# Optimization experiments

Measured on AMD Instinct MI355X. Metric: run time of the kernel, lower is better.

## Reference

```python
import jax, jax.numpy as jnp
import numpy as np

B, S, D = 2, 2048, 1024
H, DK, DV = 16, 64, 64
DF = 4096
EPS = 1e-5


def _layer_norm(x, g, b):
    mu = jnp.mean(x, axis=-1, keepdims=True)
    var = jnp.mean((x - mu) ** 2, axis=-1, keepdims=True)
    return (x - mu) * jax.lax.rsqrt(var + EPS) * g + b


def setup_inputs() -> dict:
    key = jax.random.key(0)
    ks = jax.random.split(key, 12)
    s = lambda fan_in: 1.0 / np.sqrt(fan_in)
    return {
        "enc_input": jax.random.normal(ks[0], (B, S, D), dtype=jnp.float32),
        "wq": jax.random.uniform(ks[1], (D, H * DK), jnp.float32, -s(D), s(D)),
        "wk": jax.random.uniform(ks[2], (D, H * DK), jnp.float32, -s(D), s(D)),
        "wv": jax.random.uniform(ks[3], (D, H * DV), jnp.float32, -s(D), s(D)),
        "wo": jax.random.uniform(ks[4], (H * DV, D), jnp.float32, -s(H * DV), s(H * DV)),
        "w1": jax.random.uniform(ks[5], (D, DF), jnp.float32, -s(D), s(D)),
        "b1": jax.random.uniform(ks[6], (DF,), jnp.float32, -s(D), s(D)),
        "w2": jax.random.uniform(ks[7], (DF, D), jnp.float32, -s(DF), s(DF)),
        "b2": jax.random.uniform(ks[8], (D,), jnp.float32, -s(DF), s(DF)),
        "ln1_g": jnp.ones((D,), jnp.float32),
        "ln1_b": jnp.zeros((D,), jnp.float32),
        "ln2_g": jnp.ones((D,), jnp.float32),
        "ln2_b": jnp.zeros((D,), jnp.float32),
    }


def reference(enc_input, wq, wk, wv, wo, w1, b1, w2, b2, ln1_g, ln1_b, ln2_g, ln2_b):
    x = enc_input
    # QKV projections -> [B, H, S, d]
    q = (x @ wq).reshape(B, S, H, DK).transpose(0, 2, 1, 3)
    k = (x @ wk).reshape(B, S, H, DK).transpose(0, 2, 1, 3)
    v = (x @ wv).reshape(B, S, H, DV).transpose(0, 2, 1, 3)
    # scaled dot-product attention (scale = 1/sqrt(d_k), dropout is identity at eval)
    score = jnp.einsum("bhqd,bhkd->bhqk", q, k) / jnp.sqrt(jnp.float32(DK))
    attn = jax.nn.softmax(score, axis=-1)
    ctx = jnp.einsum("bhqk,bhkd->bhqd", attn, v)
    ctx = ctx.transpose(0, 2, 1, 3).reshape(B, S, H * DV)
    atn_out = ctx @ wo
    # Add & Norm 1
    h = _layer_norm(x + atn_out, ln1_g, ln1_b)
    # FFN
    ffn = jax.nn.relu(h @ w1 + b1) @ w2 + b2
    # Add & Norm 2
    return _layer_norm(h + ffn, ln2_g, ln2_b)
```

## Files before the change

kernel.cpp:

```cpp
#include <hip/hip_runtime.h>
#include <hip/hip_bf16.h>

typedef __bf16 bf16;
typedef __bf16 bf16x4 __attribute__((ext_vector_type(4)));
typedef __bf16 bf16x8 __attribute__((ext_vector_type(8)));
typedef float  f32x4  __attribute__((ext_vector_type(4)));

#define KB 2
#define KS 2048
#define KD 1024
#define KH 16
#define KM (KB*KS)
#define KQKVN 3072
#define KDF 4096

__device__ __forceinline__ f32x4 mfma16(bf16x8 a, bf16x8 b, f32x4 c) {
  return __builtin_amdgcn_mfma_f32_16x16x32_bf16(a, b, c, 0, 0, 0);
}

__device__ __forceinline__ void g2l16(const bf16* g, bf16* l) {
  __builtin_amdgcn_global_load_lds(
      (const __attribute__((address_space(1))) unsigned int*)g,
      (__attribute__((address_space(3))) unsigned int*)l, 16, 0, 0);
}

__global__ __launch_bounds__(256) void cvt_bf16_kernel(const float* __restrict__ in,
                                                       bf16* __restrict__ out, int n) {
  int i = (blockIdx.x * 256 + threadIdx.x) * 4;
  if (i >= n) return;
  f32x4 v = *reinterpret_cast<const f32x4*>(in + i);
  bf16x4 o;
  o[0] = (bf16)v[0]; o[1] = (bf16)v[1]; o[2] = (bf16)v[2]; o[3] = (bf16)v[3];
  *reinterpret_cast<bf16x4*>(out + i) = o;
}

__global__ __launch_bounds__(256) void wtrans_kernel(const float* __restrict__ W,
                                                     bf16* __restrict__ WT,
                                                     int K, int N) {
  __shared__ float tile[32][33];
  const int n0 = blockIdx.x * 32, k0 = blockIdx.y * 32;
  const int tx = threadIdx.x & 31, ty = threadIdx.x >> 5;
#pragma unroll
  for (int j = ty; j < 32; j += 8) tile[j][tx] = W[(size_t)(k0 + j) * N + n0 + tx];
  __syncthreads();
#pragma unroll
  for (int j = ty; j < 32; j += 8) WT[(size_t)(n0 + j) * K + k0 + tx] = (bf16)tile[tx][j];
}

__global__ __launch_bounds__(256) void kvpack_kernel(const bf16* __restrict__ qkv,
                                                     bf16* __restrict__ kp,
                                                     bf16* __restrict__ vt) {
  __shared__ bf16 tile[64][72];
  const int s0 = blockIdx.x * 64;
  const int bh = blockIdx.y;
  const int b = bh >> 4, h = bh & 15;
  const int t = threadIdx.x;
  const int r = t >> 3, c8 = (t & 7) * 8;
#pragma unroll
  for (int rr = r; rr < 64; rr += 32) {
    const size_t grow = (size_t)(b * KS + s0 + rr) * KQKVN + h * 64 + c8;
    bf16x8 kv = *reinterpret_cast<const bf16x8*>(&qkv[grow + 1024]);
    *reinterpret_cast<bf16x8*>(&kp[((size_t)bh * KS + s0 + rr) * 64 + c8]) = kv;
    bf16x8 vv = *reinterpret_cast<const bf16x8*>(&qkv[grow + 2048]);
#pragma unroll
    for (int j = 0; j < 8; j++) tile[rr][c8 + j] = vv[j];
  }
  __syncthreads();
#pragma unroll
  for (int dd = r; dd < 64; dd += 32) {
    bf16x8 v;
#pragma unroll
    for (int j = 0; j < 8; j++) {
      const int pi = c8 + j;
      v[j] = tile[((pi & 3) << 4) + (pi >> 2)][dd];
    }
    *reinterpret_cast<bf16x8*>(&vt[(size_t)bh * 64 * KS + (size_t)dd * KS + s0 + c8]) = v;
  }
}

struct P4 { bf16* p[4]; };

template <typename OUT_T, bool RELU, bool HAS_BIAS, bool SPLITK>
__global__ __launch_bounds__(512, 2) void gemm256(const bf16* __restrict__ A,
                                                  const bf16* __restrict__ BT,
                                                  OUT_T* __restrict__ C, P4 pr,
                                                  const float* __restrict__ bias,
                                                  int M, int N, int K, int Kslice) {
  extern __shared__ __align__(16) bf16 sm[];
  const int tid = threadIdx.x, lane = tid & 63, w = tid >> 6;
  const int wr = w >> 2, wc = w & 3;
  const int gx = gridDim.x;
  const int nwg = gx * gridDim.y;
  int flat = blockIdx.y * gx + blockIdx.x;
  flat = (flat & 7) * (nwg >> 3) + (flat >> 3);
  const int bn = (flat % gx) * 256;
  const int bm = (flat / gx) * 256;
  const int z = blockIdx.z;
  const int NT = (SPLITK ? Kslice : K) >> 5;
  const int lr = lane & 15, hi = lane >> 4;
  int srow[2], scol[2];
#pragma unroll
  for (int j = 0; j < 2; j++) {
    const int u = j * 512 + tid;
    srow[j] = u >> 2;
    scol[j] = (((u & 3) ^ ((u >> 2) & 3))) * 8;
  }
  const bf16* Abase = A + (size_t)bm * K + (SPLITK ? z * Kslice : 0);
  const bf16* Bbase = BT + (size_t)bn * K + (SPLITK ? z * Kslice : 0);
  auto stage = [&](int t) {
    bf16* dst = sm + (size_t)(t & 3) * 16384;
    const int k0 = t * 32;
#pragma unroll
    for (int j = 0; j < 2; j++) {
      g2l16(Abase + (size_t)srow[j] * K + k0 + scol[j], dst + (j * 512 + w * 64) * 8);
      g2l16(Bbase + (size_t)srow[j] * K + k0 + scol[j],
            dst + 8192 + (j * 512 + w * 64) * 8);
    }
  };
  f32x4 acc[8][4] = {};
  stage(0); stage(1); stage(2);
  for (int t = 0; t < NT; t++) {
    const int rem = NT - 1 - t;
    if (rem >= 2)      asm volatile("s_waitcnt vmcnt(8)" ::: "memory");
    else if (rem == 1) asm volatile("s_waitcnt vmcnt(4)" ::: "memory");
    else               asm volatile("s_waitcnt vmcnt(0)" ::: "memory");
    __builtin_amdgcn_sched_barrier(0);
    __builtin_amdgcn_s_barrier();
    __builtin_amdgcn_sched_barrier(0);
    if (t + 3 < NT) stage(t + 3);
    const bf16* sa = sm + (size_t)(t & 3) * 16384;
    const bf16* sb = sa + 8192;
    bf16x8 af[8], bfr[4];
#pragma unroll
    for (int mf = 0; mf < 8; mf++) {
      const int row = wr * 128 + mf * 16 + lr;
      af[mf] = *(const bf16x8*)&sa[row * 32 + ((hi ^ (row & 3)) * 8)];
    }
#pragma unroll
    for (int nf = 0; nf < 4; nf++) {
      const int row = wc * 64 + nf * 16 + lr;
      bfr[nf] = *(const bf16x8*)&sb[row * 32 + ((hi ^ (row & 3)) * 8)];
    }
    __builtin_amdgcn_s_setprio(1);
#pragma unroll
    for (int mf = 0; mf < 8; mf++)
#pragma unroll
      for (int nf = 0; nf < 4; nf++)
        acc[mf][nf] = mfma16(af[mf], bfr[nf], acc[mf][nf]);
    __builtin_amdgcn_s_setprio(0);
  }
  const int rg = hi * 4, cl = lr;
  if (SPLITK) {
    bf16* P = pr.p[z];
#pragma unroll
    for (int mf = 0; mf < 8; mf++)
#pragma unroll
      for (int nf = 0; nf < 4; nf++) {
        const int col = bn + wc * 64 + nf * 16 + cl;
#pragma unroll
        for (int i = 0; i < 4; i++) {
          const int row = bm + wr * 128 + mf * 16 + rg + i;
          P[(size_t)row * N + col] = (bf16)acc[mf][nf][i];
        }
      }
  } else {
#pragma unroll
    for (int mf = 0; mf < 8; mf++)
#pragma unroll
      for (int nf = 0; nf < 4; nf++) {
        const int col = bn + wc * 64 + nf * 16 + cl;
        float bv = 0.f;
        if (HAS_BIAS) bv = bias[col];
#pragma unroll
        for (int i = 0; i < 4; i++) {
          const int row = bm + wr * 128 + mf * 16 + rg + i;
          float v = acc[mf][nf][i] + bv;
          if (RELU) v = fmaxf(v, 0.f);
          C[(size_t)row * N + col] = (OUT_T)v;
        }
      }
  }
}

__global__ __launch_bounds__(256) void ffn2_reduce_kernel(const bf16* __restrict__ p0,
                                                          const bf16* __restrict__ p1,
                                                          const bf16* __restrict__ p2,
                                                          const bf16* __restrict__ p3,
                                                          const float* __restrict__ b2,
                                                          float* __restrict__ out) {
  const size_t i = ((size_t)blockIdx.x * 256 + threadIdx.x) * 8;
  bf16x8 a0 = *(const bf16x8*)(p0 + i);
  bf16x8 a1 = *(const bf16x8*)(p1 + i);
  bf16x8 a2 = *(const bf16x8*)(p2 + i);
  bf16x8 a3 = *(const bf16x8*)(p3 + i);
  const int col = (int)(i & (KD - 1));
  f32x4 b0 = *(const f32x4*)(b2 + col);
  f32x4 b1 = *(const f32x4*)(b2 + col + 4);
  f32x4 o0, o1;
#pragma unroll
  for (int j = 0; j < 4; j++)
    o0[j] = (float)a0[j] + (float)a1[j] + (float)a2[j] + (float)a3[j] + b0[j];
#pragma unroll
  for (int j = 0; j < 4; j++)
    o1[j] = (float)a0[j + 4] + (float)a1[j + 4] + (float)a2[j + 4] + (float)a3[j + 4] + b1[j];
  *(f32x4*)(out + i) = o0;
  *(f32x4*)(out + i + 4) = o1;
}

template <typename OUT_T, bool RELU, bool HAS_BIAS, int BN>
__global__ __launch_bounds__(256) void gemm_bt(const bf16* __restrict__ A,
                                               const bf16* __restrict__ BT,
                                               OUT_T* __restrict__ C,
                                               const float* __restrict__ bias,
                                               int M, int N, int K) {
  constexpr int NF = BN / 32;
  __shared__ __align__(16) bf16 sa[2][128 * 32];
  __shared__ __align__(16) bf16 sb[2][BN * 32];
  const int t = threadIdx.x, lane = t & 63, w = t >> 6;
  const int gx = gridDim.x;
  const int nwg = gx * gridDim.y;
  int flat = blockIdx.y * gx + blockIdx.x;
  if ((nwg & 7) == 0) flat = (flat & 7) * (nwg >> 3) + (flat >> 3);
  const int bn = (flat % gx) * BN;
  const int bm = (flat / gx) * 128;
  const int wr = w >> 1, wc = w & 1;
  const int wcol = wc * (BN / 2);
  const int lr = lane & 15, lk = (lane >> 4) * 8;
  const int srow = w * 16 + (lane >> 2);
  const int scol = (lane & 3) * 8;
  f32x4 acc[4][NF] = {};
  const int NT = K >> 5;
  auto stage = [&](int kt, int buf) {
#pragma unroll
    for (int i = 0; i < 2; i++)
      g2l16(A + (size_t)(bm + i * 64 + srow) * K + kt * 32 + scol,
            &sa[buf][(i * 64 + w * 16) * 32]);
#pragma unroll
    for (int i = 0; i < BN / 64; i++)
      g2l16(BT + (size_t)(bn + i * 64 + srow) * K + kt * 32 + scol,
            &sb[buf][(i * 64 + w * 16) * 32]);
  };
  stage(0, 0);
  int cur = 0;
  for (int kt = 0; kt < NT; kt++) {
    __syncthreads();
    if (kt + 1 < NT) stage(kt + 1, cur ^ 1);
    bf16x8 af[4], bfr[NF];
#pragma unroll
    for (int m = 0; m < 4; m++)
      af[m] = *(const bf16x8*)&sa[cur][(wr * 64 + m * 16 + lr) * 32 + lk];
#pragma unroll
    for (int n = 0; n < NF; n++)
      bfr[n] = *(const bf16x8*)&sb[cur][(wcol + n * 16 + lr) * 32 + lk];
#pragma unroll
    for (int m = 0; m < 4; m++)
#pragma unroll
      for (int n = 0; n < NF; n++)
        acc[m][n] = mfma16(af[m], bfr[n], acc[m][n]);
    cur ^= 1;
  }
  const int rg = (lane >> 4) * 4, cl = lane & 15;
#pragma unroll
  for (int m = 0; m < 4; m++)
#pragma unroll
    for (int n = 0; n < NF; n++) {
      const int col = bn + wcol + n * 16 + cl;
      float bv = 0.f;
      if (HAS_BIAS) bv = bias[col];
#pragma unroll
      for (int i = 0; i < 4; i++) {
        const int row = bm + wr * 64 + m * 16 + rg + i;
        float v = acc[m][n][i] + bv;
        if (RELU) v = fmaxf(v, 0.f);
        C[(size_t)row * N + col] = (OUT_T)v;
      }
    }
}

__global__ __launch_bounds__(256) void attn_kernel(const bf16* __restrict__ qkv,
                                                   const bf16* __restrict__ kp,
                                                   const bf16* __restrict__ vt,
                                                   bf16* __restrict__ ctx) {
  __shared__ __align__(16) bf16 ksm[4][64 * 64];
  __shared__ __align__(16) bf16 vsm[4][64 * 64];
  __shared__ __align__(16) bf16 psm[4][32 * 64];
  const int t = threadIdx.x, lane = t & 63, w = t >> 6;
  const int flat = blockIdx.y * 16 + blockIdx.x;
  const int xcd = flat & 7, jj = flat >> 3;
  const int bh = xcd + 8 * (jj >> 4);
  const int qb = jj & 15;
  const int b = bh >> 4, h = bh & 15;
  const int qbase = qb * 128 + w * 32;
  const int lr = lane & 15, hi = lane >> 4;
  const int lk = hi * 8, rg = hi * 4, cl = lr;

  bf16x8 aq[2][2];
#pragma unroll
  for (int m = 0; m < 2; m++)
#pragma unroll
    for (int kk = 0; kk < 2; kk++) {
      bf16x8 v = *reinterpret_cast<const bf16x8*>(
          &qkv[(size_t)(b * KS + qbase + m * 16 + lr) * KQKVN + h * 64 + kk * 32 + lk]);
#pragma unroll
      for (int e = 0; e < 8; e++) v[e] = (bf16)((float)v[e] * 0.125f);
      aq[m][kk] = v;
    }

  const bf16* kpb = kp + (size_t)bh * KS * 64;
  const bf16* vtb = vt + (size_t)bh * 64 * KS;

  auto stageKV = [&](int tt) {
    const int kt0 = tt * 64;
    bf16* kd = &ksm[tt & 3][0];
    bf16* vd = &vsm[tt & 3][0];
#pragma unroll
    for (int i = 0; i < 2; i++) {
      const int q = i * 4096 + w * 1024 + (lane << 4);
      const int row = q >> 7;
      const int slot = ((q >> 4) & 7) ^ (row & 7);
      g2l16(kpb + (size_t)(kt0 + row) * 64 + slot * 8, kd + ((i * 4096 + w * 1024) >> 1));
      g2l16(vtb + (size_t)row * KS + kt0 + slot * 8,   vd + ((i * 4096 + w * 1024) >> 1));
    }
  };

  f32x4 accd[2][4] = {};
  float lsum[2][4] = {};

  stageKV(0); stageKV(1); stageKV(2);
  char* pb = (char*)&psm[w][0];
  const int NT = KS / 64;
  for (int tt = 0; tt < NT; tt++) {
    const int rem = NT - 1 - tt;
    if (rem >= 2)      asm volatile("s_waitcnt vmcnt(8)" ::: "memory");
    else if (rem == 1) asm volatile("s_waitcnt vmcnt(4)" ::: "memory");
    else               asm volatile("s_waitcnt vmcnt(0)" ::: "memory");
    __builtin_amdgcn_sched_barrier(0);
    __builtin_amdgcn_s_barrier();
    __builtin_amdgcn_sched_barrier(0);
    if (tt + 3 < NT) stageKV(tt + 3);
    const char* kb = (const char*)&ksm[tt & 3][0];
    const char* vb = (const char*)&vsm[tt & 3][0];
    bf16x8 bk[4][2];
#pragma unroll
    for (int n = 0; n < 4; n++)
#pragma unroll
      for (int kk = 0; kk < 2; kk++) {
        const int row = n * 16 + lr;
        bk[n][kk] = *(const bf16x8*)(kb + row * 128 +
                                     ((kk * 64 + hi * 16) ^ ((row & 7) << 4)));
      }
    f32x4 sc[2][4] = {};
    __builtin_amdgcn_s_setprio(1);
#pragma unroll
    for (int m = 0; m < 2; m++)
#pragma unroll
      for (int n = 0; n < 4; n++)
#pragma unroll
        for (int kk = 0; kk < 2; kk++)
          sc[m][n] = mfma16(aq[m][kk], bk[n][kk], sc[m][n]);
    __builtin_amdgcn_s_setprio(0);
#pragma unroll
    for (int m = 0; m < 2; m++)
#pragma unroll
      for (int i = 0; i < 4; i++) {
        bf16x4 pk;
#pragma unroll
        for (int n = 0; n < 4; n++) {
          const float p = __expf(sc[m][n][i]);
          lsum[m][i] += p;
          pk[n] = (bf16)p;
        }
        const int row = m * 16 + rg + i;
        *(bf16x4*)(pb + row * 128 + ((cl * 8) ^ ((row & 7) << 4))) = pk;
      }
    bf16x8 ap[2][2];
#pragma unroll
    for (int m = 0; m < 2; m++)
#pragma unroll
      for (int kk = 0; kk < 2; kk++) {
        const int row = m * 16 + lr;
        ap[m][kk] = *(const bf16x8*)(pb + row * 128 +
                                     ((kk * 64 + hi * 16) ^ ((row & 7) << 4)));
      }
    bf16x8 bv[4][2];
#pragma unroll
    for (int dt = 0; dt < 4; dt++)
#pragma unroll
      for (int kk = 0; kk < 2; kk++) {
        const int row = dt * 16 + lr;
        bv[dt][kk] = *(const bf16x8*)(vb + row * 128 +
                                      ((kk * 64 + hi * 16) ^ ((row & 7) << 4)));
      }
    __builtin_amdgcn_s_setprio(1);
#pragma unroll
    for (int m = 0; m < 2; m++)
#pragma unroll
      for (int dt = 0; dt < 4; dt++)
#pragma unroll
        for (int kk = 0; kk < 2; kk++)
          accd[m][dt] = mfma16(ap[m][kk], bv[dt][kk], accd[m][dt]);
    __builtin_amdgcn_s_setprio(0);
  }
  float rs_[2][4];
#pragma unroll
  for (int m = 0; m < 2; m++)
#pragma unroll
    for (int i = 0; i < 4; i++) {
      float s = lsum[m][i];
#pragma unroll
      for (int off = 1; off < 16; off <<= 1) s += __shfl_xor(s, off, 64);
      rs_[m][i] = 1.0f / s;
    }
#pragma unroll
  for (int m = 0; m < 2; m++)
#pragma unroll
    for (int dt = 0; dt < 4; dt++)
#pragma unroll
      for (int i = 0; i < 4; i++)
        ctx[(size_t)(b * KS + qbase + m * 16 + rg + i) * KD + h * 64 + dt * 16 + cl] =
            (bf16)(accd[m][dt][i] * rs_[m][i]);
}

template <bool ABF, bool OBF>
__global__ __launch_bounds__(256) void ln_kernel(const void* __restrict__ aptr,
                                                 const float* __restrict__ bsum,
                                                 const float* __restrict__ g,
                                                 const float* __restrict__ bet,
                                                 void* __restrict__ outp) {
  const int row = blockIdx.x;
  const int t = threadIdx.x;
  const int lane = t & 63, wid = t >> 6;
  float v[4];
  {
    f32x4 bv = *reinterpret_cast<const f32x4*>(&bsum[(size_t)row * KD + t * 4]);
    if (ABF) {
      bf16x4 av = *reinterpret_cast<const bf16x4*>(
          (const bf16*)aptr + (size_t)row * KD + t * 4);
#pragma unroll
      for (int j = 0; j < 4; j++) v[j] = (float)av[j] + bv[j];
    } else {
      f32x4 av = *reinterpret_cast<const f32x4*>(
          (const float*)aptr + (size_t)row * KD + t * 4);
#pragma unroll
      for (int j = 0; j < 4; j++) v[j] = av[j] + bv[j];
    }
  }
  float s = 0.f, s2 = 0.f;
#pragma unroll
  for (int j = 0; j < 4; j++) { s += v[j]; s2 += v[j] * v[j]; }
#pragma unroll
  for (int off = 32; off; off >>= 1) {
    s += __shfl_xor(s, off, 64);
    s2 += __shfl_xor(s2, off, 64);
  }
  __shared__ float red[8];
  if (lane == 0) { red[wid] = s; red[wid + 4] = s2; }
  __syncthreads();
  s = red[0] + red[1] + red[2] + red[3];
  s2 = red[4] + red[5] + red[6] + red[7];
  const float mu = s * (1.f / KD);
  const float var = s2 * (1.f / KD) - mu * mu;
  const float rs = rsqrtf(var + 1e-5f);
  if (OBF) {
    bf16x4 o;
#pragma unroll
    for (int j = 0; j < 4; j++)
      o[j] = (bf16)((v[j] - mu) * rs * g[t * 4 + j] + bet[t * 4 + j]);
    *reinterpret_cast<bf16x4*>((bf16*)outp + (size_t)row * KD + t * 4) = o;
  } else {
    f32x4 o;
#pragma unroll
    for (int j = 0; j < 4; j++)
      o[j] = (v[j] - mu) * rs * g[t * 4 + j] + bet[t * 4 + j];
    *reinterpret_cast<f32x4*>((float*)outp + (size_t)row * KD + t * 4) = o;
  }
}

extern "C" void kernel_launch(void* const* d_in, const int* in_sizes, int n_in,
                              void* d_out, int out_size, void* d_ws, size_t ws_size,
                              hipStream_t stream) {
  const float* x     = (const float*)d_in[0];
  const float* wq    = (const float*)d_in[1];
  const float* wk    = (const float*)d_in[2];
  const float* wv    = (const float*)d_in[3];
  const float* wo    = (const float*)d_in[4];
  const float* w1    = (const float*)d_in[5];
  const float* b1    = (const float*)d_in[6];
  const float* w2    = (const float*)d_in[7];
  const float* b2    = (const float*)d_in[8];
  const float* ln1g  = (const float*)d_in[9];
  const float* ln1b  = (const float*)d_in[10];
  const float* ln2g  = (const float*)d_in[11];
  const float* ln2b  = (const float*)d_in[12];
  float* out = (float*)d_out;

  char* ws = (char*)d_ws;
  bf16*  x_bf   = (bf16*)(ws + 0);
  bf16*  wqkvT  = (bf16*)(ws + 8388608);
  bf16*  woT    = (bf16*)(ws + 14680064);
  bf16*  w1T    = (bf16*)(ws + 16777216);
  bf16*  w2T    = (bf16*)(ws + 25165824);
  bf16*  qkv    = (bf16*)(ws + 33554432);
  bf16*  kp     = (bf16*)(ws + 58720256);
  bf16*  vt     = (bf16*)(ws + 67108864);
  float* proj   = (float*)(ws + 75497472);
  bf16*  ctx    = x_bf;
  bf16*  h_bf   = (bf16*)(ws + 8388608);
  bf16*  ffn1   = qkv;
  float* ffn2   = (float*)(ws + 33554432);
  P4 pr;
  pr.p[0] = (bf16*)(ws + 0);
  pr.p[1] = (bf16*)(ws + 16777216);
  pr.p[2] = (bf16*)(ws + 67108864);
  pr.p[3] = (bf16*)(ws + 75497472);
  P4 pzero = {};

  cvt_bf16_kernel<<<dim3(KM * KD / 1024), 256, 0, stream>>>(x, x_bf, KM * KD);
  wtrans_kernel<<<dim3(32, 32), 256, 0, stream>>>(wq, wqkvT, KD, KD);
  wtrans_kernel<<<dim3(32, 32), 256, 0, stream>>>(wk, wqkvT + 1024 * 1024, KD, KD);
  wtrans_kernel<<<dim3(32, 32), 256, 0, stream>>>(wv, wqkvT + 2048 * 1024, KD, KD);
  wtrans_kernel<<<dim3(32, 32), 256, 0, stream>>>(wo, woT, KD, KD);
  wtrans_kernel<<<dim3(128, 32), 256, 0, stream>>>(w1, w1T, KD, KDF);
  wtrans_kernel<<<dim3(32, 128), 256, 0, stream>>>(w2, w2T, KDF, KD);

  gemm256<bf16, false, false, false>
      <<<dim3(KQKVN / 256, KM / 256, 1), 512, 131072, stream>>>(
      x_bf, wqkvT, qkv, pzero, nullptr, KM, KQKVN, KD, KD);

  kvpack_kernel<<<dim3(KS / 64, KB * KH), 256, 0, stream>>>(qkv, kp, vt);

  attn_kernel<<<dim3(KS / 128, KB * KH), 256, 0, stream>>>(qkv, kp, vt, ctx);

  gemm_bt<float, false, false, 64><<<dim3(KD / 64, KM / 128), 256, 0, stream>>>(
      ctx, woT, proj, nullptr, KM, KD, KD);

  ln_kernel<false, true><<<dim3(KM), 256, 0, stream>>>(x, proj, ln1g, ln1b, h_bf);

  gemm256<bf16, true, true, false>
      <<<dim3(KDF / 256, KM / 256, 1), 512, 131072, stream>>>(
      h_bf, w1T, ffn1, pzero, b1, KM, KDF, KD, KD);

  gemm256<bf16, false, false, true>
      <<<dim3(KD / 256, KM / 256, 4), 512, 131072, stream>>>(
      ffn1, w2T, (bf16*)nullptr, pr, nullptr, KM, KD, KDF, KDF / 4);

  ffn2_reduce_kernel<<<dim3(KM * KD / 8 / 256), 256, 0, stream>>>(
      pr.p[0], pr.p[1], pr.p[2], pr.p[3], b2, ffn2);

  ln_kernel<true, false><<<dim3(KM), 256, 0, stream>>>(h_bf, ffn2, ln2g, ln2b, out);
}
```

Measured before the change: 250.2 us.

## Keep attention probabilities in registers and use split-K 256 GEMM for output projection

The attention kernel computes scores transposed (K as the A operand), so the exponentiated probabilities already sit in the right MFMA operand layout. They are packed straight into registers, which removes the per-wave LDS round trip for P, and the V transpose permutation in kvpack is changed to match. The row-sum reduction now needs fewer shuffles. Separately, the output projection moves from the smaller gemm_bt kernel to the 256-tile split-K gemm256 plus a generic reduce4 kernel, trading extra bf16 partial writes and a reduction pass for better MFMA tile efficiency.

```diff
diff --git a/kernel.cpp b/kernel.cpp
--- a/kernel.cpp
+++ b/kernel.cpp
@@ -72,7 +72,9 @@
 #pragma unroll
     for (int j = 0; j < 8; j++) {
       const int pi = c8 + j;
-      v[j] = tile[((pi & 3) << 4) + (pi >> 2)][dd];
+      const int key = ((pi >> 5) << 5) | (((pi >> 2) & 1) << 4) |
+                      (((pi >> 3) & 3) << 2) | (pi & 3);
+      v[j] = tile[key][dd];
     }
     *reinterpret_cast<bf16x8*>(&vt[(size_t)bh * 64 * KS + (size_t)dd * KS + s0 + c8]) = v;
   }
@@ -182,99 +184,34 @@
   }
 }
 
-__global__ __launch_bounds__(256) void ffn2_reduce_kernel(const bf16* __restrict__ p0,
-                                                          const bf16* __restrict__ p1,
-                                                          const bf16* __restrict__ p2,
-                                                          const bf16* __restrict__ p3,
-                                                          const float* __restrict__ b2,
-                                                          float* __restrict__ out) {
+template <bool BIAS>
+__global__ __launch_bounds__(256) void reduce4_kernel(const bf16* __restrict__ p0,
+                                                      const bf16* __restrict__ p1,
+                                                      const bf16* __restrict__ p2,
+                                                      const bf16* __restrict__ p3,
+                                                      const float* __restrict__ bias,
+                                                      float* __restrict__ out) {
   const size_t i = ((size_t)blockIdx.x * 256 + threadIdx.x) * 8;
   bf16x8 a0 = *(const bf16x8*)(p0 + i);
   bf16x8 a1 = *(const bf16x8*)(p1 + i);
   bf16x8 a2 = *(const bf16x8*)(p2 + i);
   bf16x8 a3 = *(const bf16x8*)(p3 + i);
-  const int col = (int)(i & (KD - 1));
-  f32x4 b0 = *(const f32x4*)(b2 + col);
-  f32x4 b1 = *(const f32x4*)(b2 + col + 4);
   f32x4 o0, o1;
 #pragma unroll
   for (int j = 0; j < 4; j++)
-    o0[j] = (float)a0[j] + (float)a1[j] + (float)a2[j] + (float)a3[j] + b0[j];
+    o0[j] = (float)a0[j] + (float)a1[j] + (float)a2[j] + (float)a3[j];
 #pragma unroll
   for (int j = 0; j < 4; j++)
-    o1[j] = (float)a0[j + 4] + (float)a1[j + 4] + (float)a2[j + 4] + (float)a3[j + 4] + b1[j];
+    o1[j] = (float)a0[j + 4] + (float)a1[j + 4] + (float)a2[j + 4] + (float)a3[j + 4];
+  if (BIAS) {
+    const int col = (int)(i & (KD - 1));
+    f32x4 b0 = *(const f32x4*)(bias + col);
+    f32x4 b1 = *(const f32x4*)(bias + col + 4);
+#pragma unroll
+    for (int j = 0; j < 4; j++) { o0[j] += b0[j]; o1[j] += b1[j]; }
+  }
   *(f32x4*)(out + i) = o0;
   *(f32x4*)(out + i + 4) = o1;
-}
-
-template <typename OUT_T, bool RELU, bool HAS_BIAS, int BN>
-__global__ __launch_bounds__(256) void gemm_bt(const bf16* __restrict__ A,
-                                               const bf16* __restrict__ BT,
-                                               OUT_T* __restrict__ C,
-                                               const float* __restrict__ bias,
-                                               int M, int N, int K) {
-  constexpr int NF = BN / 32;
-  __shared__ __align__(16) bf16 sa[2][128 * 32];
-  __shared__ __align__(16) bf16 sb[2][BN * 32];
-  const int t = threadIdx.x, lane = t & 63, w = t >> 6;
-  const int gx = gridDim.x;
-  const int nwg = gx * gridDim.y;
-  int flat = blockIdx.y * gx + blockIdx.x;
-  if ((nwg & 7) == 0) flat = (flat & 7) * (nwg >> 3) + (flat >> 3);
-  const int bn = (flat % gx) * BN;
-  const int bm = (flat / gx) * 128;
-  const int wr = w >> 1, wc = w & 1;
-  const int wcol = wc * (BN / 2);
-  const int lr = lane & 15, lk = (lane >> 4) * 8;
-  const int srow = w * 16 + (lane >> 2);
-  const int scol = (lane & 3) * 8;
-  f32x4 acc[4][NF] = {};
-  const int NT = K >> 5;
-  auto stage = [&](int kt, int buf) {
-#pragma unroll
-    for (int i = 0; i < 2; i++)
-      g2l16(A + (size_t)(bm + i * 64 + srow) * K + kt * 32 + scol,
-            &sa[buf][(i * 64 + w * 16) * 32]);
-#pragma unroll
-    for (int i = 0; i < BN / 64; i++)
-      g2l16(BT + (size_t)(bn + i * 64 + srow) * K + kt * 32 + scol,
-            &sb[buf][(i * 64 + w * 16) * 32]);
-  };
-  stage(0, 0);
-  int cur = 0;
-  for (int kt = 0; kt < NT; kt++) {
-    __syncthreads();
-    if (kt + 1 < NT) stage(kt + 1, cur ^ 1);
-    bf16x8 af[4], bfr[NF];
-#pragma unroll
-    for (int m = 0; m < 4; m++)
-      af[m] = *(const bf16x8*)&sa[cur][(wr * 64 + m * 16 + lr) * 32 + lk];
-#pragma unroll
-    for (int n = 0; n < NF; n++)
-      bfr[n] = *(const bf16x8*)&sb[cur][(wcol + n * 16 + lr) * 32 + lk];
-#pragma unroll
-    for (int m = 0; m < 4; m++)
-#pragma unroll
-      for (int n = 0; n < NF; n++)
-        acc[m][n] = mfma16(af[m], bfr[n], acc[m][n]);
-    cur ^= 1;
-  }
-  const int rg = (lane >> 4) * 4, cl = lane & 15;
-#pragma unroll
-  for (int m = 0; m < 4; m++)
-#pragma unroll
-    for (int n = 0; n < NF; n++) {
-      const int col = bn + wcol + n * 16 + cl;
-      float bv = 0.f;
-      if (HAS_BIAS) bv = bias[col];
-#pragma unroll
-      for (int i = 0; i < 4; i++) {
-        const int row = bm + wr * 64 + m * 16 + rg + i;
-        float v = acc[m][n][i] + bv;
-        if (RELU) v = fmaxf(v, 0.f);
-        C[(size_t)row * N + col] = (OUT_T)v;
-      }
-    }
 }
 
 __global__ __launch_bounds__(256) void attn_kernel(const bf16* __restrict__ qkv,
@@ -283,7 +220,6 @@
                                                    bf16* __restrict__ ctx) {
   __shared__ __align__(16) bf16 ksm[4][64 * 64];
   __shared__ __align__(16) bf16 vsm[4][64 * 64];
-  __shared__ __align__(16) bf16 psm[4][32 * 64];
   const int t = threadIdx.x, lane = t & 63, w = t >> 6;
   const int flat = blockIdx.y * 16 + blockIdx.x;
   const int xcd = flat & 7, jj = flat >> 3;
@@ -324,10 +260,9 @@
   };
 
   f32x4 accd[2][4] = {};
-  float lsum[2][4] = {};
+  float lsum[2] = {};
 
   stageKV(0); stageKV(1); stageKV(2);
-  char* pb = (char*)&psm[w][0];
   const int NT = KS / 64;
   for (int tt = 0; tt < NT; tt++) {
     const int rem = NT - 1 - tt;
@@ -357,31 +292,27 @@
       for (int n = 0; n < 4; n++)
 #pragma unroll
         for (int kk = 0; kk < 2; kk++)
-          sc[m][n] = mfma16(aq[m][kk], bk[n][kk], sc[m][n]);
+          sc[m][n] = mfma16(bk[n][kk], aq[m][kk], sc[m][n]);
     __builtin_amdgcn_s_setprio(0);
-#pragma unroll
-    for (int m = 0; m < 2; m++)
-#pragma unroll
-      for (int i = 0; i < 4; i++) {
-        bf16x4 pk;
-#pragma unroll
-        for (int n = 0; n < 4; n++) {
-          const float p = __expf(sc[m][n][i]);
-          lsum[m][i] += p;
-          pk[n] = (bf16)p;
+    bf16x8 pa[2][2];
+#pragma unroll
+    for (int m = 0; m < 2; m++) {
+      float p[4][4];
+#pragma unroll
+      for (int n = 0; n < 4; n++)
+#pragma unroll
+        for (int i = 0; i < 4; i++) {
+          p[n][i] = __expf(sc[m][n][i]);
+          lsum[m] += p[n][i];
         }
-        const int row = m * 16 + rg + i;
-        *(bf16x4*)(pb + row * 128 + ((cl * 8) ^ ((row & 7) << 4))) = pk;
+#pragma unroll
+      for (int kk = 0; kk < 2; kk++) {
+        bf16x8 v;
+#pragma unroll
+        for (int j = 0; j < 8; j++) v[j] = (bf16)p[kk * 2 + (j >> 2)][j & 3];
+        pa[m][kk] = v;
       }
-    bf16x8 ap[2][2];
-#pragma unroll
-    for (int m = 0; m < 2; m++)
-#pragma unroll
-      for (int kk = 0; kk < 2; kk++) {
-        const int row = m * 16 + lr;
-        ap[m][kk] = *(const bf16x8*)(pb + row * 128 +
-                                     ((kk * 64 + hi * 16) ^ ((row & 7) << 4)));
-      }
+    }
     bf16x8 bv[4][2];
 #pragma unroll
     for (int dt = 0; dt < 4; dt++)
@@ -398,19 +329,23 @@
       for (int dt = 0; dt < 4; dt++)
 #pragma unroll
         for (int kk = 0; kk < 2; kk++)
-          accd[m][dt] = mfma16(ap[m][kk], bv[dt][kk], accd[m][dt]);
+          accd[m][dt] = mfma16(pa[m][kk], bv[dt][kk], accd[m][dt]);
     __builtin_amdgcn_s_setprio(0);
   }
+  float tot[2];
+#pragma unroll
+  for (int m = 0; m < 2; m++) {
+    float s = lsum[m];
+    s += __shfl_xor(s, 16, 64);
+    s += __shfl_xor(s, 32, 64);
+    tot[m] = s;
+  }
   float rs_[2][4];
 #pragma unroll
   for (int m = 0; m < 2; m++)
 #pragma unroll
-    for (int i = 0; i < 4; i++) {
-      float s = lsum[m][i];
-#pragma unroll
-      for (int off = 1; off < 16; off <<= 1) s += __shfl_xor(s, off, 64);
-      rs_[m][i] = 1.0f / s;
-    }
+    for (int i = 0; i < 4; i++)
+      rs_[m][i] = 1.0f / __shfl(tot[m], rg + i, 64);
 #pragma unroll
   for (int m = 0; m < 2; m++)
 #pragma unroll
@@ -508,6 +443,11 @@
   bf16*  h_bf   = (bf16*)(ws + 8388608);
   bf16*  ffn1   = qkv;
   float* ffn2   = (float*)(ws + 33554432);
+  P4 wp;
+  wp.p[0] = (bf16*)(ws + 33554432);
+  wp.p[1] = (bf16*)(ws + 41943040);
+  wp.p[2] = (bf16*)(ws + 58720256);
+  wp.p[3] = (bf16*)(ws + 67108864);
   P4 pr;
   pr.p[0] = (bf16*)(ws + 0);
   pr.p[1] = (bf16*)(ws + 16777216);
@@ -531,8 +471,11 @@
 
   attn_kernel<<<dim3(KS / 128, KB * KH), 256, 0, stream>>>(qkv, kp, vt, ctx);
 
-  gemm_bt<float, false, false, 64><<<dim3(KD / 64, KM / 128), 256, 0, stream>>>(
-      ctx, woT, proj, nullptr, KM, KD, KD);
+  gemm256<bf16, false, false, true>
+      <<<dim3(KD / 256, KM / 256, 4), 512, 131072, stream>>>(
+      ctx, woT, (bf16*)nullptr, wp, nullptr, KM, KD, KD, KD / 4);
+  reduce4_kernel<false><<<dim3(KM * KD / 8 / 256), 256, 0, stream>>>(
+      wp.p[0], wp.p[1], wp.p[2], wp.p[3], nullptr, proj);
 
   ln_kernel<false, true><<<dim3(KM), 256, 0, stream>>>(x, proj, ln1g, ln1b, h_bf);
 
@@ -543,8 +486,7 @@
   gemm256<bf16, false, false, true>
       <<<dim3(KD / 256, KM / 256, 4), 512, 131072, stream>>>(
       ffn1, w2T, (bf16*)nullptr, pr, nullptr, KM, KD, KDF, KDF / 4);
-
-  ffn2_reduce_kernel<<<dim3(KM * KD / 8 / 256), 256, 0, stream>>>(
+  reduce4_kernel<true><<<dim3(KM * KD / 8 / 256), 256, 0, stream>>>(
       pr.p[0], pr.p[1], pr.p[2], pr.p[3], b2, ffn2);
 
   ln_kernel<true, false><<<dim3(KM), 256, 0, stream>>>(h_bf, ffn2, ln2g, ln2b, out);
```

Result: no change. 251.6 us (+0.6%).
